# Optimization experiments

Hardware: AMD Instinct MI355X
Metric: run time of the kernel (lower is better)

## Reference

```python
import jax, jax.numpy as jnp
import numpy as np

D_MODEL = 1024
NUM_HEADS = 16
D_K = D_MODEL // NUM_HEADS


def setup_inputs() -> dict:
    key = jax.random.key(0)
    kq, kk, kv, k1, k2, k3, k4 = jax.random.split(key, 7)
    B, S = 2, 2048
    # Xavier-uniform init for square [d_model, d_model] weights
    limit = float(np.sqrt(6.0 / (D_MODEL + D_MODEL)))
    def xav(k):
        return jax.random.uniform(k, (D_MODEL, D_MODEL), jnp.float32, -limit, limit)
    return {
        "query": jax.random.normal(kq, (B, S, D_MODEL), jnp.float32),
        "key": jax.random.normal(kk, (B, S, D_MODEL), jnp.float32),
        "value": jax.random.normal(kv, (B, S, D_MODEL), jnp.float32),
        "W_q": xav(k1),
        "W_k": xav(k2),
        "W_v": xav(k3),
        "W_o": xav(k4),
    }


def reference(query, key, value, W_q, W_k, W_v, W_o):
    B, Sq, _ = query.shape
    Sk = key.shape[1]
    # Linear layers: y = x @ W.T (torch nn.Linear convention)
    Q = (query @ W_q.T).reshape(B, Sq, NUM_HEADS, D_K).transpose(0, 2, 1, 3)
    K = (key @ W_k.T).reshape(B, Sk, NUM_HEADS, D_K).transpose(0, 2, 1, 3)
    V = (value @ W_v.T).reshape(B, Sk, NUM_HEADS, D_K).transpose(0, 2, 1, 3)
    scale = 1.0 / jnp.sqrt(jnp.asarray(D_K, Q.dtype))
    scores = jnp.einsum("bhqd,bhkd->bhqk", Q, K) * scale  # [B,H,Sq,Sk]
    attn = jax.nn.softmax(scores, axis=-1)
    # dropout is identity in eval mode
    out = jnp.einsum("bhqk,bhkd->bhqd", attn, V)
    out = out.transpose(0, 2, 1, 3).reshape(B, Sq, D_MODEL)
    return out @ W_o.T
```

## Files before the change

kernel.cpp:

```cpp
#include <hip/hip_runtime.h>
#include <math.h>

typedef unsigned short ushort_t;
typedef __attribute__((ext_vector_type(8))) short short8;
typedef __attribute__((ext_vector_type(4))) float f32x4;
typedef __attribute__((ext_vector_type(16))) float f32x16;
typedef __attribute__((ext_vector_type(4))) unsigned short ushort4v;
typedef __attribute__((ext_vector_type(2))) unsigned int uint2v;
typedef __attribute__((ext_vector_type(4))) unsigned int uint4v;

#define D_MODEL 1024
#define SEQ 2048
#define MROWS 4096
#define PLANE (MROWS * D_MODEL)
#define WELEM (D_MODEL * D_MODEL)

static __device__ __forceinline__ ushort_t f2bf(float f) {
    unsigned u = __builtin_bit_cast(unsigned, f);
    return (ushort_t)((u + 0x7fffu + ((u >> 16) & 1u)) >> 16);
}
static __device__ __forceinline__ unsigned cvtpk(float lo, float hi) {
    unsigned r;
    asm("v_cvt_pk_bf16_f32 %0, %1, %2" : "=v"(r) : "v"(lo), "v"(hi));
    return r;
}

#define GLDS16(gp, lp)                                                         \
    __builtin_amdgcn_global_load_lds(                                          \
        (const __attribute__((address_space(1))) void*)(gp),                   \
        (__attribute__((address_space(3))) void*)(lp), 16, 0, 0)

__global__ __launch_bounds__(256)
void cvt_all(const float* __restrict__ q, const float* __restrict__ k,
             const float* __restrict__ v, const float* __restrict__ w0,
             const float* __restrict__ w1, const float* __restrict__ w2,
             const float* __restrict__ w3, ushort_t* __restrict__ dst) {
    int blk = blockIdx.x;
    const float* s;
    size_t base;
    if (blk < 6144) {
        const int p = blk >> 11;
        s = (p == 0) ? q : (p == 1) ? k : v;
        base = (size_t)p * PLANE;
        blk &= 2047;
    } else {
        const int p = (blk - 6144) >> 9;
        s = (p == 0) ? w0 : (p == 1) ? w1 : (p == 2) ? w2 : w3;
        base = 3 * (size_t)PLANE + (size_t)p * WELEM;
        blk = (blk - 6144) & 511;
    }
    const int i = (blk * 256 + threadIdx.x) * 8;
    float4 a = *(const float4*)(s + i);
    float4 bb = *(const float4*)(s + i + 4);
    short8 o;
    o[0] = (short)f2bf(a.x); o[1] = (short)f2bf(a.y);
    o[2] = (short)f2bf(a.z); o[3] = (short)f2bf(a.w);
    o[4] = (short)f2bf(bb.x); o[5] = (short)f2bf(bb.y);
    o[6] = (short)f2bf(bb.z); o[7] = (short)f2bf(bb.w);
    *(short8*)(dst + base + i) = o;
}

__global__ __launch_bounds__(256)
void gemm3(const ushort_t* __restrict__ Xq, const ushort_t* __restrict__ Wb,
           ushort_t* __restrict__ Cb) {
    __shared__ __align__(16) ushort_t As[128 * 64];
    __shared__ __align__(16) ushort_t Bs[128 * 64];

    const int lin = blockIdx.x + blockIdx.y * 8 + blockIdx.z * 256;
    const int lin2 = (lin & 7) * 96 + (lin >> 3);
    const int z = lin2 >> 8;
    const int rem = lin2 & 255;
    const int by = rem >> 3;
    const int bx = rem & 7;

    const ushort_t* A = Xq + (size_t)z * PLANE;
    const ushort_t* B = Wb + (size_t)z * WELEM;
    ushort_t* C = Cb + (size_t)z * PLANE;

    const int tid = threadIdx.x;
    const int lane = tid & 63;
    const int wid = tid >> 6;
    const int wr = wid >> 1, wc = wid & 1;
    const int brow = by * 128;
    const int bcol = bx * 128;

    const int lrow = lane >> 3;
    const int loff = ((lane & 7) ^ lrow) * 8;

    const ushort_t* aS[4];
    const ushort_t* bS[4];
#pragma unroll
    for (int i = 0; i < 4; ++i) {
        aS[i] = A + (size_t)(brow + wid * 32 + i * 8 + lrow) * D_MODEL + loff;
        bS[i] = B + (size_t)(bcol + wid * 32 + i * 8 + lrow) * D_MODEL + loff;
    }

    f32x4 acc[4][4];
#pragma unroll
    for (int i = 0; i < 4; ++i)
#pragma unroll
        for (int j = 0; j < 4; ++j) acc[i][j] = {0.f, 0.f, 0.f, 0.f};

    const int fr = lane & 15, fg = lane >> 4;

    for (int k0 = 0; k0 < D_MODEL; k0 += 64) {
        __syncthreads();
#pragma unroll
        for (int i = 0; i < 4; ++i) {
            GLDS16(aS[i] + k0, As + (wid * 32 + i * 8) * 64);
            GLDS16(bS[i] + k0, Bs + (wid * 32 + i * 8) * 64);
        }
        __syncthreads();
#pragma unroll
        for (int ks = 0; ks < 2; ++ks) {
            const int coff = (ks * 32 + fg * 8) ^ ((fr & 7) << 3);
            short8 af[4], bw[4];
#pragma unroll
            for (int mi = 0; mi < 4; ++mi)
                af[mi] = *(const short8*)&As[(wr * 64 + mi * 16 + fr) * 64 + coff];
#pragma unroll
            for (int nj = 0; nj < 4; ++nj)
                bw[nj] = *(const short8*)&Bs[(wc * 64 + nj * 16 + fr) * 64 + coff];
#pragma unroll
            for (int mi = 0; mi < 4; ++mi)
#pragma unroll
                for (int nj = 0; nj < 4; ++nj)
                    acc[mi][nj] = __builtin_amdgcn_mfma_f32_16x16x32_bf16(
                        af[mi], bw[nj], acc[mi][nj], 0, 0, 0);
        }
    }

    if (z < 2) {
#pragma unroll
        for (int mi = 0; mi < 4; ++mi)
#pragma unroll
            for (int nj = 0; nj < 4; ++nj) {
                const int n = bcol + wc * 64 + nj * 16 + fr;
#pragma unroll
                for (int r = 0; r < 4; ++r) {
                    const int m = brow + wr * 64 + mi * 16 + fg * 4 + r;
                    C[(size_t)m * D_MODEL + n] = f2bf(acc[mi][nj][r]);
                }
            }
    } else {
#pragma unroll
        for (int mi = 0; mi < 4; ++mi)
#pragma unroll
            for (int nj = 0; nj < 4; ++nj) {
                const int n = bcol + wc * 64 + nj * 16 + fr;
                const int m0 = brow + wr * 64 + mi * 16 + fg * 4;
                ushort4v o4;
#pragma unroll
                for (int r = 0; r < 4; ++r) o4[r] = f2bf(acc[mi][nj][r]);
                *(ushort4v*)&C[((size_t)(m0 >> 11) << 21) + (size_t)n * SEQ + (m0 & 2047)] = o4;
            }
    }
}

__global__ __launch_bounds__(256)
void gemm_out(const ushort_t* __restrict__ A, const ushort_t* __restrict__ B,
              float* __restrict__ C) {
    __shared__ __align__(16) ushort_t As[2][128 * 64];
    __shared__ __align__(16) ushort_t Bs[2][64 * 64];

    const int lin = blockIdx.x + blockIdx.y * 16;
    const int lin2 = (lin & 7) * 64 + (lin >> 3);
    const int by = lin2 >> 4;
    const int bx = lin2 & 15;

    const int tid = threadIdx.x;
    const int lane = tid & 63;
    const int wid = tid >> 6;
    const int wr = wid >> 1, wc = wid & 1;
    const int brow = by * 128;
    const int bcol = bx * 64;

    const int lrow = lane >> 3;
    const int loff = ((lane & 7) ^ lrow) * 8;

    const ushort_t* aSrc[4];
    const ushort_t* bSrc[2];
#pragma unroll
    for (int i = 0; i < 4; ++i)
        aSrc[i] = A + (size_t)(brow + (wid * 4 + i) * 8 + lrow) * D_MODEL + loff;
#pragma unroll
    for (int i = 0; i < 2; ++i)
        bSrc[i] = B + (size_t)(bcol + (wid * 2 + i) * 8 + lrow) * D_MODEL + loff;

    f32x4 acc[4][2];
#pragma unroll
    for (int i = 0; i < 4; ++i)
#pragma unroll
        for (int j = 0; j < 2; ++j) acc[i][j] = {0.f, 0.f, 0.f, 0.f};

    const int fr = lane & 15, fg = lane >> 4;

#pragma unroll
    for (int i = 0; i < 4; ++i) GLDS16(aSrc[i], As[0] + (wid * 4 + i) * 512);
#pragma unroll
    for (int i = 0; i < 2; ++i) GLDS16(bSrc[i], Bs[0] + (wid * 2 + i) * 512);

    int cur = 0;
    for (int k0 = 0; k0 < D_MODEL; k0 += 64) {
        __syncthreads();
        if (k0 + 64 < D_MODEL) {
#pragma unroll
            for (int i = 0; i < 4; ++i)
                GLDS16(aSrc[i] + k0 + 64, As[cur ^ 1] + (wid * 4 + i) * 512);
#pragma unroll
            for (int i = 0; i < 2; ++i)
                GLDS16(bSrc[i] + k0 + 64, Bs[cur ^ 1] + (wid * 2 + i) * 512);
        }
#pragma unroll
        for (int ks = 0; ks < 2; ++ks) {
            const int coff = (ks * 32 + fg * 8) ^ ((fr & 7) << 3);
            short8 af[4], bw[2];
#pragma unroll
            for (int mi = 0; mi < 4; ++mi)
                af[mi] = *(const short8*)&As[cur][(wr * 64 + mi * 16 + fr) * 64 + coff];
#pragma unroll
            for (int nj = 0; nj < 2; ++nj)
                bw[nj] = *(const short8*)&Bs[cur][(wc * 32 + nj * 16 + fr) * 64 + coff];
#pragma unroll
            for (int mi = 0; mi < 4; ++mi)
#pragma unroll
                for (int nj = 0; nj < 2; ++nj)
                    acc[mi][nj] = __builtin_amdgcn_mfma_f32_16x16x32_bf16(
                        af[mi], bw[nj], acc[mi][nj], 0, 0, 0);
        }
        cur ^= 1;
    }

#pragma unroll
    for (int mi = 0; mi < 4; ++mi)
#pragma unroll
        for (int nj = 0; nj < 2; ++nj) {
            const int n = bcol + wc * 32 + nj * 16 + fr;
#pragma unroll
            for (int r = 0; r < 4; ++r) {
                const int m = brow + wr * 64 + mi * 16 + fg * 4 + r;
                C[(size_t)m * D_MODEL + n] = acc[mi][nj][r];
            }
        }
}

__global__ __launch_bounds__(512, 4)
void attn_mfma(const ushort_t* __restrict__ Qp, const ushort_t* __restrict__ Kp,
               const ushort_t* __restrict__ VT, ushort_t* __restrict__ Ap) {
    __shared__ __align__(16) ushort_t KB[4][4096];
    __shared__ __align__(16) ushort_t VB[4][4096];
    __shared__ float sm[2][128];
    __shared__ float sl[2][128];

    const int tid = threadIdx.x;
    const int lane = tid & 63;
    const int wid = tid >> 6;
    const int qgrp = wid & 3;
    const int khalf = wid >> 2;

    const int bid0 = blockIdx.x;
    const int bid = (bid0 & 7) * 64 + (bid0 >> 3);
    const int qt = bid & 15;
    const int h = (bid >> 4) & 15;
    const int b = bid >> 8;

    const int lrow = lane >> 3;
    const int loff = ((lane & 7) ^ lrow) * 8;
    const int q31 = lane & 31;
    const int hi = lane >> 5;

    const int m0 = b * SEQ + qt * 128;

    ushort_t* Qstage = &KB[2][0];
#pragma unroll
    for (int j = 0; j < 2; ++j) {
        const ushort_t* qS =
            Qp + (size_t)(m0 + wid * 16 + j * 8 + lrow) * D_MODEL + h * 64 + loff;
        GLDS16(qS, Qstage + (wid * 16 + j * 8) * 64);
    }
    const ushort_t* kS =
        Kp + (size_t)(b * SEQ + wid * 8 + lrow) * D_MODEL + h * 64 + loff;
    const ushort_t* vS =
        VT + ((size_t)b << 21) + (size_t)(h * 64 + wid * 8 + lrow) * SEQ + loff;
    GLDS16(kS, KB[0] + wid * 512);
    GLDS16(vS, VB[0] + wid * 512);
    kS += 64 * D_MODEL;
    vS += 64;
    GLDS16(kS, KB[1] + wid * 512);
    GLDS16(vS, VB[1] + wid * 512);
    kS += 64 * D_MODEL;
    vS += 64;
    __syncthreads();

    const int qrow = qgrp * 32 + q31;
    const int rsw = q31 & 7;
    short8 aq[4];
#pragma unroll
    for (int s = 0; s < 4; ++s)
        aq[s] = *(const short8*)&Qstage[qrow * 64 + (((s * 2 + hi) ^ rsw) * 8)];
    __syncthreads();

    f32x16 accO[2];
#pragma unroll
    for (int db = 0; db < 2; ++db)
#pragma unroll
        for (int r = 0; r < 16; ++r) accO[db][r] = 0.f;
    float m_s = -INFINITY;
    float l_p = 0.f;

    const float CEXP = 0.18033688011112042f;
    const int kbase = khalf * 32;

    int cur = 0;
    for (int st = 0; st < SEQ / 128; ++st) {
        if (st + 1 < SEQ / 128) {
            const int b0 = (cur ^ 1) * 2;
            GLDS16(kS, KB[b0] + wid * 512);
            GLDS16(vS, VB[b0] + wid * 512);
            kS += 64 * D_MODEL;
            vS += 64;
            GLDS16(kS, KB[b0 + 1] + wid * 512);
            GLDS16(vS, VB[b0 + 1] + wid * 512);
            kS += 64 * D_MODEL;
            vS += 64;
        }

#pragma unroll
        for (int sub = 0; sub < 2; ++sub) {
            const int bufi = cur * 2 + sub;

            f32x16 accS;
#pragma unroll
            for (int r = 0; r < 16; ++r) accS[r] = 0.f;
            __builtin_amdgcn_s_setprio(1);
#pragma unroll
            for (int s = 0; s < 4; ++s) {
                short8 ak = *(const short8*)&KB[bufi][(kbase + q31) * 64 +
                                                     (((s * 2 + hi) ^ rsw) * 8)];
                accS = __builtin_amdgcn_mfma_f32_32x32x16_bf16(ak, aq[s], accS, 0, 0, 0);
            }
            __builtin_amdgcn_s_setprio(0);

            float mx = accS[0];
#pragma unroll
            for (int r = 1; r < 16; ++r) mx = fmaxf(mx, accS[r]);
            mx = fmaxf(mx, __shfl_xor(mx, 32));
            const float cand = mx * CEXP;
            if (__any(cand > m_s + 8.f)) {
                const float mnew = fmaxf(m_s, cand);
                const float al = __builtin_amdgcn_exp2f(m_s - mnew);
                m_s = mnew;
                l_p *= al;
#pragma unroll
                for (int db = 0; db < 2; ++db)
#pragma unroll
                    for (int r = 0; r < 16; ++r) accO[db][r] *= al;
            }
            float ps = 0.f;
            const float nm = -m_s;
#pragma unroll
            for (int r = 0; r < 16; ++r) {
                const float p = __builtin_amdgcn_exp2f(fmaf(accS[r], CEXP, nm));
                accS[r] = p;
                ps += p;
            }
            l_p += ps;

            short8 pf[2];
#pragma unroll
            for (int ks2 = 0; ks2 < 2; ++ks2) {
                const int bse = ks2 * 8;
                unsigned w0 = cvtpk(accS[bse + 0], accS[bse + 1]);
                unsigned w1 = cvtpk(accS[bse + 2], accS[bse + 3]);
                unsigned w2 = cvtpk(accS[bse + 4], accS[bse + 5]);
                unsigned w3 = cvtpk(accS[bse + 6], accS[bse + 7]);
                asm("v_permlane32_swap_b32 %0, %1" : "+v"(w0), "+v"(w2));
                asm("v_permlane32_swap_b32 %0, %1" : "+v"(w1), "+v"(w3));
                uint4v u = {w0, w1, w2, w3};
                pf[ks2] = __builtin_bit_cast(short8, u);
            }

            __builtin_amdgcn_s_setprio(1);
#pragma unroll
            for (int db = 0; db < 2; ++db)
#pragma unroll
                for (int ks2 = 0; ks2 < 2; ++ks2) {
                    short8 av = *(const short8*)&VB[bufi][(db * 32 + q31) * 64 +
                        (((khalf * 4 + ks2 * 2 + hi) ^ rsw) * 8)];
                    accO[db] = __builtin_amdgcn_mfma_f32_32x32x16_bf16(
                        av, pf[ks2], accO[db], 0, 0, 0);
                }
            __builtin_amdgcn_s_setprio(0);
        }
        cur ^= 1;
        __syncthreads();
    }

    const float lt = l_p + __shfl_xor(l_p, 32);
    const int qg = qgrp * 32 + q31;
    if (lane < 32) {
        sm[khalf][qg] = m_s;
        sl[khalf][qg] = lt;
    }
    __syncthreads();
    const float mA = sm[0][qg], mB = sm[1][qg];
    const float mC = fmaxf(mA, mB);
    const float wA = __builtin_amdgcn_exp2f(mA - mC);
    const float wB = __builtin_amdgcn_exp2f(mB - mC);
    const float inv = 1.0f / (wA * sl[0][qg] + wB * sl[1][qg]);

    float* O1 = (float*)KB;
    if (khalf == 1) {
#pragma unroll
        for (int db = 0; db < 2; ++db)
#pragma unroll
            for (int rq = 0; rq < 4; ++rq) {
                f32x4 v;
#pragma unroll
                for (int j = 0; j < 4; ++j) v[j] = accO[db][rq * 4 + j] * wB;
                const int c = db * 8 + rq * 2 + hi;
                *(f32x4*)&O1[qg * 64 + ((c ^ (q31 & 15)) * 4)] = v;
            }
    }
    __syncthreads();
    unsigned* QsW = (unsigned*)VB;
    if (khalf == 0) {
        const int kkw = 2 * (q31 & 15);
#pragma unroll
        for (int db = 0; db < 2; ++db)
#pragma unroll
            for (int rq = 0; rq < 4; ++rq) {
                const int c = db * 8 + rq * 2 + hi;
                f32x4 o1 = *(const f32x4*)&O1[qg * 64 + ((c ^ (q31 & 15)) * 4)];
                float o0 = (accO[db][rq * 4 + 0] * wA + o1[0]) * inv;
                float o1v = (accO[db][rq * 4 + 1] * wA + o1[1]) * inv;
                float o2 = (accO[db][rq * 4 + 2] * wA + o1[2]) * inv;
                float o3 = (accO[db][rq * 4 + 3] * wA + o1[3]) * inv;
                uint2v u = {cvtpk(o0, o1v), cvtpk(o2, o3)};
                const int c0 = 4 * rq + 2 * hi + 16 * db;
                *(uint2v*)&QsW[qg * 32 + (c0 ^ kkw)] = u;
            }
    }
    __syncthreads();
#pragma unroll
    for (int pass = 0; pass < 2; ++pass) {
        const int r = wid * 16 + pass * 8 + (lane >> 3);
        const int g8 = lane & 7;
        const int kk = 2 * (r & 15);
        uint2v u0 = *(const uint2v*)&QsW[r * 32 + ((4 * g8) ^ kk)];
        uint2v u1 = *(const uint2v*)&QsW[r * 32 + ((4 * g8 + 2) ^ kk)];
        uint4v o = {u0[0], u0[1], u1[0], u1[1]};
        *(uint4v*)&Ap[(size_t)(m0 + r) * D_MODEL + h * 64 + g8 * 8] = o;
    }
}

extern "C" void kernel_launch(void* const* d_in, const int* in_sizes, int n_in,
                              void* d_out, int out_size, void* d_ws, size_t ws_size,
                              hipStream_t stream) {
    const float* query = (const float*)d_in[0];
    const float* key   = (const float*)d_in[1];
    const float* value = (const float*)d_in[2];
    const float* W_q   = (const float*)d_in[3];
    const float* W_k   = (const float*)d_in[4];
    const float* W_v   = (const float*)d_in[5];
    const float* W_o   = (const float*)d_in[6];
    float* out = (float*)d_out;

    ushort_t* ws = (ushort_t*)d_ws;
    ushort_t* Xq = ws;
    ushort_t* Wb = ws + 3 * (size_t)PLANE;
    ushort_t* Qp = ws + 4 * (size_t)PLANE;
    ushort_t* Kp = Qp + (size_t)PLANE;
    ushort_t* VT = Kp + (size_t)PLANE;
    ushort_t* Ap = VT + (size_t)PLANE;

    cvt_all<<<8192, 256, 0, stream>>>(query, key, value, W_q, W_k, W_v, W_o, Xq);

    dim3 g3(D_MODEL / 128, MROWS / 128, 3);
    gemm3<<<g3, 256, 0, stream>>>(Xq, Wb, Qp);

    attn_mfma<<<512, 512, 0, stream>>>(Qp, Kp, VT, Ap);

    dim3 go(D_MODEL / 64, MROWS / 128);
    gemm_out<<<go, 256, 0, stream>>>(Ap, Wb + 3 * (size_t)WELEM, out);
}
```

Before: 123.3 us.

## Fuse fp32-to-bf16 activation conversion into QKV projection GEMM

Stops converting query/key/value to bf16 in a separate pass. The QKV GEMM now loads fp32 activations into registers, converts them with packed bf16 instructions, and writes them to LDS, prefetching the next k-tile during the current iteration. The weight-only conversion kernel also switches to the packed conversion instruction. This removes a full write and re-read of the bf16 activation planes, at the cost of reading twice as many bytes per A tile inside the GEMM, extra register pressure, and synchronous stores in place of async global-to-LDS loads. The packed convert may also round differently from the previous manual code.

```diff
diff --git a/kernel.cpp b/kernel.cpp
--- a/kernel.cpp
+++ b/kernel.cpp
@@ -24,6 +24,11 @@
     asm("v_cvt_pk_bf16_f32 %0, %1, %2" : "=v"(r) : "v"(lo), "v"(hi));
     return r;
 }
+static __device__ __forceinline__ short8 cvt8(float4 a, float4 b) {
+    uint4v u = {cvtpk(a.x, a.y), cvtpk(a.z, a.w),
+                cvtpk(b.x, b.y), cvtpk(b.z, b.w)};
+    return __builtin_bit_cast(short8, u);
+}
 
 #define GLDS16(gp, lp)                                                         \
     __builtin_amdgcn_global_load_lds(                                          \
@@ -31,37 +36,20 @@
         (__attribute__((address_space(3))) void*)(lp), 16, 0, 0)
 
 __global__ __launch_bounds__(256)
-void cvt_all(const float* __restrict__ q, const float* __restrict__ k,
-             const float* __restrict__ v, const float* __restrict__ w0,
-             const float* __restrict__ w1, const float* __restrict__ w2,
-             const float* __restrict__ w3, ushort_t* __restrict__ dst) {
-    int blk = blockIdx.x;
-    const float* s;
-    size_t base;
-    if (blk < 6144) {
-        const int p = blk >> 11;
-        s = (p == 0) ? q : (p == 1) ? k : v;
-        base = (size_t)p * PLANE;
-        blk &= 2047;
-    } else {
-        const int p = (blk - 6144) >> 9;
-        s = (p == 0) ? w0 : (p == 1) ? w1 : (p == 2) ? w2 : w3;
-        base = 3 * (size_t)PLANE + (size_t)p * WELEM;
-        blk = (blk - 6144) & 511;
-    }
-    const int i = (blk * 256 + threadIdx.x) * 8;
+void cvt_w(const float* __restrict__ w0, const float* __restrict__ w1,
+           const float* __restrict__ w2, const float* __restrict__ w3,
+           ushort_t* __restrict__ dst) {
+    const int p = blockIdx.x >> 9;
+    const float* s = (p == 0) ? w0 : (p == 1) ? w1 : (p == 2) ? w2 : w3;
+    const int i = (((int)blockIdx.x & 511) * 256 + threadIdx.x) * 8;
     float4 a = *(const float4*)(s + i);
     float4 bb = *(const float4*)(s + i + 4);
-    short8 o;
-    o[0] = (short)f2bf(a.x); o[1] = (short)f2bf(a.y);
-    o[2] = (short)f2bf(a.z); o[3] = (short)f2bf(a.w);
-    o[4] = (short)f2bf(bb.x); o[5] = (short)f2bf(bb.y);
-    o[6] = (short)f2bf(bb.z); o[7] = (short)f2bf(bb.w);
-    *(short8*)(dst + base + i) = o;
+    *(short8*)(dst + (size_t)p * WELEM + i) = cvt8(a, bb);
 }
 
 __global__ __launch_bounds__(256)
-void gemm3(const ushort_t* __restrict__ Xq, const ushort_t* __restrict__ Wb,
+void gemm3(const float* __restrict__ Xq, const float* __restrict__ Xk,
+           const float* __restrict__ Xv, const ushort_t* __restrict__ Wb,
            ushort_t* __restrict__ Cb) {
     __shared__ __align__(16) ushort_t As[128 * 64];
     __shared__ __align__(16) ushort_t Bs[128 * 64];
@@ -73,7 +61,7 @@
     const int by = rem >> 3;
     const int bx = rem & 7;
 
-    const ushort_t* A = Xq + (size_t)z * PLANE;
+    const float* A = (z == 0) ? Xq : (z == 1) ? Xk : Xv;
     const ushort_t* B = Wb + (size_t)z * WELEM;
     ushort_t* C = Cb + (size_t)z * PLANE;
 
@@ -85,13 +73,14 @@
     const int bcol = bx * 128;
 
     const int lrow = lane >> 3;
-    const int loff = ((lane & 7) ^ lrow) * 8;
-
-    const ushort_t* aS[4];
+    const int g8 = lane & 7;
+    const int loff = (g8 ^ lrow) * 8;
+
+    const float* aF[4];
     const ushort_t* bS[4];
 #pragma unroll
     for (int i = 0; i < 4; ++i) {
-        aS[i] = A + (size_t)(brow + wid * 32 + i * 8 + lrow) * D_MODEL + loff;
+        aF[i] = A + (size_t)(brow + wid * 32 + i * 8 + lrow) * D_MODEL + loff;
         bS[i] = B + (size_t)(bcol + wid * 32 + i * 8 + lrow) * D_MODEL + loff;
     }
 
@@ -102,13 +91,28 @@
         for (int j = 0; j < 4; ++j) acc[i][j] = {0.f, 0.f, 0.f, 0.f};
 
     const int fr = lane & 15, fg = lane >> 4;
+
+    float4 ar[4][2];
+#pragma unroll
+    for (int i = 0; i < 4; ++i) {
+        ar[i][0] = *(const float4*)(aF[i]);
+        ar[i][1] = *(const float4*)(aF[i] + 4);
+    }
 
     for (int k0 = 0; k0 < D_MODEL; k0 += 64) {
         __syncthreads();
 #pragma unroll
         for (int i = 0; i < 4; ++i) {
-            GLDS16(aS[i] + k0, As + (wid * 32 + i * 8) * 64);
+            *(short8*)&As[(wid * 32 + i * 8 + lrow) * 64 + g8 * 8] =
+                cvt8(ar[i][0], ar[i][1]);
             GLDS16(bS[i] + k0, Bs + (wid * 32 + i * 8) * 64);
+        }
+        if (k0 + 64 < D_MODEL) {
+#pragma unroll
+            for (int i = 0; i < 4; ++i) {
+                ar[i][0] = *(const float4*)(aF[i] + k0 + 64);
+                ar[i][1] = *(const float4*)(aF[i] + k0 + 68);
+            }
         }
         __syncthreads();
 #pragma unroll
@@ -467,17 +471,16 @@
     float* out = (float*)d_out;
 
     ushort_t* ws = (ushort_t*)d_ws;
-    ushort_t* Xq = ws;
     ushort_t* Wb = ws + 3 * (size_t)PLANE;
     ushort_t* Qp = ws + 4 * (size_t)PLANE;
     ushort_t* Kp = Qp + (size_t)PLANE;
     ushort_t* VT = Kp + (size_t)PLANE;
     ushort_t* Ap = VT + (size_t)PLANE;
 
-    cvt_all<<<8192, 256, 0, stream>>>(query, key, value, W_q, W_k, W_v, W_o, Xq);
+    cvt_w<<<2048, 256, 0, stream>>>(W_q, W_k, W_v, W_o, Wb);
 
     dim3 g3(D_MODEL / 128, MROWS / 128, 3);
-    gemm3<<<g3, 256, 0, stream>>>(Xq, Wb, Qp);
+    gemm3<<<g3, 256, 0, stream>>>(query, key, value, Wb, Qp);
 
     attn_mfma<<<512, 512, 0, stream>>>(Qp, Kp, VT, Ap);
 
```

Result: faster. 119.7 us, median of 2 (-2.9%).
